# Kernel optimization log

Measured on AMD Instinct MI355X. Metric: run time of the kernel, lower is better.

## Reference

```python
import jax, jax.numpy as jnp
import numpy as np
from jax import lax

B, N, C, H, W, D, BEV = 2, 6, 64, 128, 352, 48, 64


def _make_buffers():
    # depths: linspace(1,100,D) -> used with shape (1,1,D,1)
    depths = jnp.linspace(1.0, 100.0, D).reshape(1, 1, D, 1)
    y, x = jnp.meshgrid(jnp.arange(H), jnp.arange(W), indexing='ij')
    xy1 = jnp.stack((x.flatten(), y.flatten(), jnp.ones(H * W)), axis=0).astype(jnp.float32)  # (3, H*W)
    return depths, xy1


def setup_inputs() -> dict:
    key = jax.random.key(0)
    ks = jax.random.split(key, 8)
    image_features = jax.random.normal(ks[0], (B * N, C, H, W), jnp.float32)
    # realistic invertible pinhole intrinsics embedded in 4x4
    fx = 500.0 + 10.0 * jax.random.normal(ks[1], (B, N))
    fy = 500.0 + 10.0 * jax.random.normal(ks[2], (B, N))
    K = jnp.tile(jnp.eye(4, dtype=jnp.float32), (B, N, 1, 1))
    K = K.at[..., 0, 0].set(fx).at[..., 1, 1].set(fy)
    K = K.at[..., 0, 2].set(W / 2.0).at[..., 1, 2].set(H / 2.0)
    extrinsics = jnp.tile(jnp.eye(4, dtype=jnp.float32), (B, N, 1, 1)) + 0.01 * jax.random.normal(ks[3], (B, N, 4, 4))
    view_attention = jnp.ones((1, N, 1, H, W), jnp.float32)
    depth_attention = jnp.ones((1, D, 1, 1), jnp.float32)
    # kaiming-normal conv weights (fan_in mode, relu gain sqrt(2))
    c1w = jax.random.normal(ks[4], (BEV, 3, 3, 3), jnp.float32) * np.sqrt(2.0 / (3 * 9))
    c1b = jnp.zeros((BEV,), jnp.float32)
    c2w = jax.random.normal(ks[5], (BEV, BEV, 3, 3), jnp.float32) * np.sqrt(2.0 / (BEV * 9))
    c2b = jnp.zeros((BEV,), jnp.float32)
    bn1_g = jnp.ones((BEV,), jnp.float32); bn1_b = jnp.zeros((BEV,), jnp.float32)
    bn2_g = jnp.ones((BEV,), jnp.float32); bn2_b = jnp.zeros((BEV,), jnp.float32)
    depths, xy1 = _make_buffers()
    return dict(image_features=image_features, intrinsics=K, extrinsics=extrinsics,
                view_attention=view_attention, depth_attention=depth_attention,
                c1w=c1w, c1b=c1b, bn1_g=bn1_g, bn1_b=bn1_b,
                c2w=c2w, c2b=c2b, bn2_g=bn2_g, bn2_b=bn2_b,
                depths=depths, xy1=xy1)


def _conv3x3(x, w, b):
    y = lax.conv_general_dilated(x, w, (1, 1), 'SAME',
                                 dimension_numbers=('NCHW', 'OIHW', 'NCHW'))
    return y + b.reshape(1, -1, 1, 1)


def _bn_train(x, g, b, eps=1e-5):
    # torch BatchNorm2d in training mode: biased batch stats over (B,H,W)
    m = x.mean(axis=(0, 2, 3), keepdims=True)
    v = x.var(axis=(0, 2, 3), keepdims=True)
    return g.reshape(1, -1, 1, 1) * (x - m) * lax.rsqrt(v + eps) + b.reshape(1, -1, 1, 1)


def reference(image_features, intrinsics, extrinsics, view_attention, depth_attention,
              c1w, c1b, bn1_g, bn1_b, c2w, c2b, bn2_g, bn2_b, depths, xy1):
    BN = B * N
    # ---- lift ----
    K3 = intrinsics.reshape(BN, 4, 4)[:, :3, :3]
    Kinv = jnp.linalg.inv(K3)                          # (BN,3,3)
    rays = jnp.einsum('bij,jp->bip', Kinv, xy1)        # (BN,3,H*W)
    # depths (1,1,D,1) * rays (BN,3,1,HW) -> (BN,3,D,HW), then the original's
    # .view(B,N,3,H,W,D) (a raw row-major reshape, reproduced faithfully)
    pc = (depths * rays[:, :, None, :]).reshape(B, N, 3, H, W, D)
    # (depth_probs in the original is computed then discarded; omitted)
    # ---- splat (fused weighted reduction over N and D) ----
    da = jax.nn.softmax(depth_attention, axis=1).reshape(D)       # (D,)
    va = jax.nn.softmax(view_attention, axis=1)[0, :, 0]          # (N,H,W)
    bev_features = jnp.einsum('bnchwd,d,nhw->bchw', pc, da, va)   # (B,3,H,W)
    h = jax.nn.relu(_bn_train(_conv3x3(bev_features, c1w, c1b), bn1_g, bn1_b))
    bev = jax.nn.relu(_bn_train(_conv3x3(h, c2w, c2b), bn2_g, bn2_b))
    return pc, bev
```

## Files before the change

### kernel.cpp

```cpp
#include <hip/hip_runtime.h>

#define W_ 352
#define H_ 128
#define HW 45056
#define D_ 48
#define B_ 2
#define N_ 6
#define DHW (D_*HW)
#define PC_SIZE (36*DHW)
#define BHW (B_*HW)
#define BEVN (B_*64*HW)

#define WS_KINV 0
#define WS_SUM1 192
#define WS_SQ1  256
#define WS_SUM2 448
#define WS_SQ2  512

#define NBN_BLK (BEVN/2048)
#define NPC_BLK 4224
#define PC_ITER 18

typedef unsigned short ushort_t;
typedef __attribute__((ext_vector_type(8))) short bf16x8;
typedef __attribute__((ext_vector_type(4))) float f32x4;
typedef __attribute__((ext_vector_type(8))) unsigned short u16x8;

static __device__ inline ushort_t f2bf(float f) {
    union { float f; unsigned u; } v; v.f = f;
    unsigned r = v.u + 0x7FFF + ((v.u >> 16) & 1);
    return (ushort_t)(r >> 16);
}
static __device__ inline float bf2f(ushort_t u) {
    union { unsigned u; float f; } v; v.u = ((unsigned)u) << 16; return v.f;
}
static __device__ inline void invert3x3(const float* __restrict__ M, float* __restrict__ o) {
    float a = M[0], b = M[1], c = M[2];
    float d = M[4], e = M[5], f = M[6];
    float g = M[8], h = M[9], ii = M[10];
    float det = a*(e*ii - f*h) - b*(d*ii - f*g) + c*(d*h - e*g);
    float inv = 1.f / det;
    o[0] = (e*ii - f*h)*inv; o[1] = (c*h - b*ii)*inv; o[2] = (b*f - c*e)*inv;
    o[3] = (f*g - d*ii)*inv; o[4] = (a*ii - c*g)*inv; o[5] = (c*d - a*f)*inv;
    o[6] = (d*h - e*g)*inv;  o[7] = (b*g - a*h)*inv;  o[8] = (a*e - b*d)*inv;
}

__global__ __launch_bounds__(256) void k_fused1(const float* __restrict__ K4,
                                                const float* __restrict__ datt,
                                                const float* __restrict__ vatt,
                                                const float* __restrict__ depths,
                                                const float* __restrict__ w1,
                                                const float* __restrict__ b1,
                                                const float* __restrict__ w2,
                                                float* __restrict__ ws,
                                                ushort_t* __restrict__ h1pm,
                                                ushort_t* __restrict__ packedW) {
    int bid = blockIdx.x, tid = threadIdx.x;
    if (bid >= 352) {
        int e = (bid - 352) * 256 + tid;
        int tap = e >> 12;
        int r   = e & 4095;
        int n   = r >> 6, k = r & 63;
        int slot = (k >> 3) ^ (n & 7);
        packedW[tap * 4096 + n * 64 + slot * 8 + (k & 7)] = f2bf(w2[(n * 64 + k) * 9 + tap]);
        return;
    }
    if (bid == 0 && tid >= 128 && tid < 140)
        invert3x3(K4 + (tid - 128) * 16, ws + WS_KINV + (tid - 128) * 9);

    __shared__ float sBev[3][10][34];
    __shared__ float wl[64 * 27];
    __shared__ float sDep[48], sDa[48], sKinv[54];
    __shared__ __align__(16) ushort_t sTile[256 * 64];
    __shared__ float sSum[64], sSq[64];

    int b  = bid / 176;
    int t0 = bid - b * 176;
    int ty = t0 / 11, tx = t0 - ty * 11;
    int y0 = ty * 8, x0 = tx * 32;

    if (tid < 48) sDep[tid] = depths[tid];
    if (tid < 64) { sSum[tid] = 0.f; sSq[tid] = 0.f; }
    if (tid >= 64 && tid < 70) invert3x3(K4 + (b * 6 + tid - 64) * 16, sKinv + (tid - 64) * 9);
    if (tid == 192) {
        float mx = -1e30f;
        for (int k = 0; k < D_; k++) mx = fmaxf(mx, datt[k]);
        float s = 0.f, e[D_];
        for (int k = 0; k < D_; k++) { e[k] = expf(datt[k] - mx); s += e[k]; }
        float invs = 1.f / s;
        for (int k = 0; k < D_; k++) sDa[k] = e[k] * invs;
    }
    for (int i = tid; i < 64 * 27; i += 256) wl[i] = w1[i];
    __syncthreads();

    for (int idx = tid; idx < 340; idx += 256) {
        int hy = idx / 34, hx = idx - hy * 34;
        int py = y0 + hy - 1, px = x0 + hx - 1;
        float a0 = 0.f, a1 = 0.f, a2 = 0.f;
        if ((unsigned)py < H_ && (unsigned)px < W_) {
            int pix = py * W_ + px;
            float va[N_]; float mx = -1e30f;
            for (int n = 0; n < N_; n++) { va[n] = vatt[n * HW + pix]; mx = fmaxf(mx, va[n]); }
            float s = 0.f;
            for (int n = 0; n < N_; n++) { va[n] = expf(va[n] - mx); s += va[n]; }
            float invs = 1.f / s;
            int q0 = pix * 48;
            int d = q0 / HW;
            int p = q0 - d * HW;
            int y = p / W_;
            int x = p - y * W_;
            float fx = (float)x, fy = (float)y;
            float S0 = 0.f, S1 = 0.f, S2 = 0.f;
            #pragma unroll
            for (int dd = 0; dd < D_; dd++) {
                float wq = sDa[dd] * sDep[d];
                S0 = fmaf(wq, fx, S0);
                S1 = fmaf(wq, fy, S1);
                S2 += wq;
                x++; fx += 1.f;
                if (x == W_) { x = 0; fx = 0.f; y++; fy += 1.f; if (y == H_) { y = 0; fy = 0.f; d++; } }
            }
            for (int n = 0; n < N_; n++) {
                float van = va[n] * invs;
                const float* kv = sKinv + n * 9;
                a0 = fmaf(van, fmaf(kv[0], S0, fmaf(kv[1], S1, kv[2] * S2)), a0);
                a1 = fmaf(van, fmaf(kv[3], S0, fmaf(kv[4], S1, kv[5] * S2)), a1);
                a2 = fmaf(van, fmaf(kv[6], S0, fmaf(kv[7], S1, kv[8] * S2)), a2);
            }
        }
        sBev[0][hy][hx] = a0;
        sBev[1][hy][hx] = a1;
        sBev[2][hy][hx] = a2;
    }
    __syncthreads();

    int oy = tid >> 5, ox = tid & 31;
    int y = y0 + oy, x = x0 + ox;
    float v[27];
    #pragma unroll
    for (int ci = 0; ci < 3; ci++)
        #pragma unroll
        for (int dy = 0; dy < 3; dy++)
            #pragma unroll
            for (int dx = 0; dx < 3; dx++)
                v[ci * 9 + dy * 3 + dx] = sBev[ci][oy + dy][ox + dx];
    u16x8 pack[8];
    #pragma unroll
    for (int co = 0; co < 64; co++) {
        float acc = b1[co];
        #pragma unroll
        for (int k = 0; k < 27; k++) acc = fmaf(wl[co * 27 + k], v[k], acc);
        pack[co >> 3][co & 7] = (short)f2bf(acc);
    }
    ushort_t* dst = h1pm + (size_t)(b * HW + y * W_ + x) * 64;
    #pragma unroll
    for (int j = 0; j < 8; j++) {
        *(u16x8*)(dst + j * 8) = pack[j];
        *(u16x8*)(&sTile[tid * 64 + j * 8]) = pack[j];
    }
    __syncthreads();

    int c8 = tid & 7;
    int lp = tid >> 3;
    float s[8] = {0,0,0,0,0,0,0,0}, q[8] = {0,0,0,0,0,0,0,0};
    for (int p = lp; p < 256; p += 32) {
        u16x8 vv = *(const u16x8*)(&sTile[p * 64 + c8 * 8]);
        #pragma unroll
        for (int e = 0; e < 8; e++) {
            float f = bf2f(vv[e]);
            s[e] += f;
            q[e] = fmaf(f, f, q[e]);
        }
    }
    #pragma unroll
    for (int e = 0; e < 8; e++) {
        s[e] += __shfl_xor(s[e], 8);  s[e] += __shfl_xor(s[e], 16); s[e] += __shfl_xor(s[e], 32);
        q[e] += __shfl_xor(q[e], 8);  q[e] += __shfl_xor(q[e], 16); q[e] += __shfl_xor(q[e], 32);
    }
    if ((tid & 56) == 0) {
        #pragma unroll
        for (int e = 0; e < 8; e++) {
            atomicAdd(&sSum[c8 * 8 + e], s[e]);
            atomicAdd(&sSq[c8 * 8 + e], q[e]);
        }
    }
    __syncthreads();
    if (tid < 64) {
        atomicAdd(ws + WS_SUM1 + tid, sSum[tid]);
        atomicAdd(ws + WS_SQ1 + tid, sSq[tid]);
    }
}

__global__ __launch_bounds__(256) void k_conv2(const ushort_t* __restrict__ h1pm,
                                               const ushort_t* __restrict__ packedW,
                                               const float* __restrict__ b2,
                                               const float* __restrict__ g1,
                                               const float* __restrict__ bb1,
                                               float* __restrict__ ws,
                                               float* __restrict__ h2f) {
    __shared__ __align__(16) ushort_t sA[204 * 64];
    __shared__ __align__(16) ushort_t sB[3 * 4096];
    __shared__ float sSc[64], sSh[64];
    __shared__ float sRs[4][64], sRq[4][64];

    const int tid = threadIdx.x;
    if (tid < 64) {
        const float invM = 1.f / (float)BHW;
        float m = ws[WS_SUM1 + tid] * invM;
        float var = ws[WS_SQ1 + tid] * invM - m * m;
        float sc = g1[tid] * rsqrtf(var + 1e-5f);
        sSc[tid] = sc;
        sSh[tid] = bb1[tid] - m * sc;
    }
    __syncthreads();

    const int bid = blockIdx.x;
    const int b  = bid / 352;
    const int r0 = bid - b * 352;
    const int yb = r0 / 11;
    const int xb = r0 - yb * 11;
    const int x0 = xb * 32;
    const int y0 = yb * 4;
    const ushort_t* h1p = h1pm + (size_t)b * HW * 64;

    for (int idx = tid; idx < 204 * 8; idx += 256) {
        int r  = idx >> 3;
        int c8 = idx & 7;
        int hy = r / 34;
        int hx = r - hy * 34;
        int py = y0 + hy - 1, px = x0 + hx - 1;
        u16x8 ov = {0, 0, 0, 0, 0, 0, 0, 0};
        if ((unsigned)py < H_ && (unsigned)px < W_) {
            u16x8 v = *(const u16x8*)(h1p + (size_t)(py * W_ + px) * 64 + c8 * 8);
            #pragma unroll
            for (int e = 0; e < 8; e++) {
                int ci = c8 * 8 + e;
                float f = fmaxf(fmaf(sSc[ci], bf2f(v[e]), sSh[ci]), 0.f);
                ov[e] = (short)f2bf(f);
            }
        }
        int slot = c8 ^ (r & 7);
        *(u16x8*)(&sA[r * 64 + slot * 8]) = ov;
    }

    const int w    = tid >> 6;
    const int lane = tid & 63;
    const int g    = lane >> 4;
    const int c16  = lane & 15;

    f32x4 acc[2][4];
    #pragma unroll
    for (int m = 0; m < 2; m++)
        #pragma unroll
        for (int n = 0; n < 4; n++)
            acc[m][n] = (f32x4){0.f, 0.f, 0.f, 0.f};

    for (int grp = 0; grp < 3; grp++) {
        __syncthreads();
        const uint4* src = (const uint4*)(packedW + grp * 3 * 4096);
        uint4* dst = (uint4*)sB;
        #pragma unroll
        for (int i = 0; i < 6; i++) dst[tid + 256 * i] = src[tid + 256 * i];
        __syncthreads();
        #pragma unroll
        for (int tt = 0; tt < 3; tt++) {
            bf16x8 afr[2][2];
            #pragma unroll
            for (int mrep = 0; mrep < 2; mrep++)
                #pragma unroll
                for (int kk = 0; kk < 2; kk++) {
                    int r = (w + grp) * 34 + tt + c16 + 16 * mrep;
                    int slot = (g + 4 * kk) ^ (r & 7);
                    afr[mrep][kk] = *(const bf16x8*)(&sA[r * 64 + slot * 8]);
                }
            #pragma unroll
            for (int nrep = 0; nrep < 4; nrep++) {
                int n = 16 * nrep + c16;
                #pragma unroll
                for (int kk = 0; kk < 2; kk++) {
                    int slot = (g + 4 * kk) ^ (n & 7);
                    bf16x8 bfr = *(const bf16x8*)(&sB[tt * 4096 + n * 64 + slot * 8]);
                    #pragma unroll
                    for (int mrep = 0; mrep < 2; mrep++)
                        acc[mrep][nrep] = __builtin_amdgcn_mfma_f32_16x16x32_bf16(
                            afr[mrep][kk], bfr, acc[mrep][nrep], 0, 0, 0);
                }
            }
        }
    }

    const int y = y0 + w;
    #pragma unroll
    for (int nrep = 0; nrep < 4; nrep++) {
        int co = 16 * nrep + c16;
        float bias = b2[co];
        float* dstrow = h2f + (size_t)(b * 64 + co) * HW + y * W_;
        float s = 0.f, q = 0.f;
        #pragma unroll
        for (int mrep = 0; mrep < 2; mrep++)
            #pragma unroll
            for (int j = 0; j < 4; j++) {
                float val = acc[mrep][nrep][j] + bias;
                s += val;
                q = fmaf(val, val, q);
                dstrow[x0 + 16 * mrep + g * 4 + j] = val;
            }
        s += __shfl_xor(s, 16); s += __shfl_xor(s, 32);
        q += __shfl_xor(q, 16); q += __shfl_xor(q, 32);
        if (g == 0) { sRs[w][co] = s; sRq[w][co] = q; }
    }
    __syncthreads();
    if (tid < 64) {
        float s = sRs[0][tid] + sRs[1][tid] + sRs[2][tid] + sRs[3][tid];
        float q = sRq[0][tid] + sRq[1][tid] + sRq[2][tid] + sRq[3][tid];
        atomicAdd(ws + WS_SUM2 + tid, s);
        atomicAdd(ws + WS_SQ2 + tid, q);
    }
}

__global__ __launch_bounds__(256) void k_tail(const float* __restrict__ depths,
                                              const float* __restrict__ ws,
                                              const float* __restrict__ g2,
                                              const float* __restrict__ bb2,
                                              float* __restrict__ out) {
    int bid = blockIdx.x, tid = threadIdx.x;
    if (bid >= NBN_BLK) {
        int pcbid = bid - NBN_BLK;
        for (int i = 0; i < PC_ITER; i++) {
            int ch = i * NPC_BLK + pcbid;
            int f = ch * 1024 + tid * 4;
            int bnc = f / DHW;
            int r1  = f - bnc * DHW;
            int d   = r1 / HW;
            int p   = r1 - d * HW;
            int y   = p / W_;
            int x   = p - y * W_;
            float ka = ws[WS_KINV + bnc * 3 + 0];
            float kb = ws[WS_KINV + bnc * 3 + 1];
            float kc = ws[WS_KINV + bnc * 3 + 2];
            float dep = depths[d];
            float base = fmaf(kb, (float)y, kc);
            f32x4 v;
            v.x = dep * fmaf(ka, (float)(x + 0), base);
            v.y = dep * fmaf(ka, (float)(x + 1), base);
            v.z = dep * fmaf(ka, (float)(x + 2), base);
            v.w = dep * fmaf(ka, (float)(x + 3), base);
            *(f32x4*)(out + f) = v;
        }
        return;
    }
    float* bev = out + PC_SIZE;
    int t = bid * 256 + tid;
    int f = t * 8;
    int c = (f / HW) & 63;
    const float invM = 1.f / (float)BHW;
    float m = ws[WS_SUM2 + c] * invM;
    float var = ws[WS_SQ2 + c] * invM - m * m;
    float sc = g2[c] * rsqrtf(var + 1e-5f);
    float sh = bb2[c] - m * sc;
    f32x4 a = *(f32x4*)(bev + f);
    f32x4 d = *(f32x4*)(bev + f + 4);
    a.x = fmaxf(fmaf(sc, a.x, sh), 0.f);
    a.y = fmaxf(fmaf(sc, a.y, sh), 0.f);
    a.z = fmaxf(fmaf(sc, a.z, sh), 0.f);
    a.w = fmaxf(fmaf(sc, a.w, sh), 0.f);
    d.x = fmaxf(fmaf(sc, d.x, sh), 0.f);
    d.y = fmaxf(fmaf(sc, d.y, sh), 0.f);
    d.z = fmaxf(fmaf(sc, d.z, sh), 0.f);
    d.w = fmaxf(fmaf(sc, d.w, sh), 0.f);
    *(f32x4*)(bev + f) = a;
    *(f32x4*)(bev + f + 4) = d;
}

extern "C" void kernel_launch(void* const* d_in, const int* in_sizes, int n_in,
                              void* d_out, int out_size, void* d_ws, size_t ws_size,
                              hipStream_t stream) {
    const float* K4     = (const float*)d_in[1];
    const float* vatt   = (const float*)d_in[3];
    const float* datt   = (const float*)d_in[4];
    const float* c1w    = (const float*)d_in[5];
    const float* c1b    = (const float*)d_in[6];
    const float* g1     = (const float*)d_in[7];
    const float* bb1    = (const float*)d_in[8];
    const float* c2w    = (const float*)d_in[9];
    const float* c2b    = (const float*)d_in[10];
    const float* g2     = (const float*)d_in[11];
    const float* bb2    = (const float*)d_in[12];
    const float* depths = (const float*)d_in[13];

    float* out = (float*)d_out;
    float* ws  = (float*)d_ws;
    char* base = (char*)d_out;
    ushort_t* h1pm    = (ushort_t*)base;
    ushort_t* packedW = (ushort_t*)(base + (12u << 20));
    float*    h2f     = out + PC_SIZE;

    hipMemsetAsync(ws, 0, 640 * sizeof(float), stream);
    k_fused1<<<496, 256, 0, stream>>>(K4, datt, vatt, depths, c1w, c1b, c2w, ws, h1pm, packedW);
    k_conv2 <<<704, 256, 0, stream>>>(h1pm, packedW, c2b, g1, bb1, ws, h2f);
    k_tail  <<<NBN_BLK + NPC_BLK, 256, 0, stream>>>(depths, ws, g2, bb2, out);
}
```

Measured before the change: 137.1 us.

## Store conv2 output as bf16 scratch in pc region and use nontemporal pc stores

The conv2 output is now written as bf16 into a scratch area inside the point-cloud output region instead of fp32 directly into the bev output. The tail kernel becomes one block per pc chunk: blocks overlapping the scratch first read it, apply BN+ReLU and write fp32 bev, synchronise, then overwrite their chunk with point-cloud values. Point-cloud stores use nontemporal hints. This cuts conv2 write and tail read traffic in half and removes the per-block loop, but rounds the pre-BN activations to bf16 and relies on each block reading only its own scratch chunk before overwriting it.

After: 123.2 us, median of 2. 1.11x faster.

```diff
diff --git a/kernel.cpp b/kernel.cpp
--- a/kernel.cpp
+++ b/kernel.cpp
@@ -17,14 +17,15 @@
 #define WS_SUM2 448
 #define WS_SQ2  512
 
-#define NBN_BLK (BEVN/2048)
-#define NPC_BLK 4224
-#define PC_ITER 18
+#define NPC_BLK (PC_SIZE/1024)
+#define CH_H2B0 4096
+#define CH_H2B1 (CH_H2B0 + BEVN/2048)
 
 typedef unsigned short ushort_t;
 typedef __attribute__((ext_vector_type(8))) short bf16x8;
 typedef __attribute__((ext_vector_type(4))) float f32x4;
 typedef __attribute__((ext_vector_type(8))) unsigned short u16x8;
+typedef __attribute__((ext_vector_type(4))) unsigned short u16x4;
 
 static __device__ inline ushort_t f2bf(float f) {
     union { float f; unsigned u; } v; v.f = f;
@@ -43,6 +44,29 @@
     o[0] = (e*ii - f*h)*inv; o[1] = (c*h - b*ii)*inv; o[2] = (b*f - c*e)*inv;
     o[3] = (f*g - d*ii)*inv; o[4] = (a*ii - c*g)*inv; o[5] = (c*d - a*f)*inv;
     o[6] = (d*h - e*g)*inv;  o[7] = (b*g - a*h)*inv;  o[8] = (a*e - b*d)*inv;
+}
+
+static __device__ inline void pc_write(int pcblk, const float* __restrict__ ws,
+                                       const float* __restrict__ depths,
+                                       float* __restrict__ out) {
+    int f = pcblk * 1024 + (int)threadIdx.x * 4;
+    int bnc = f / DHW;
+    int r1  = f - bnc * DHW;
+    int d   = r1 / HW;
+    int p   = r1 - d * HW;
+    int y   = p / W_;
+    int x   = p - y * W_;
+    float ka = ws[WS_KINV + bnc * 3 + 0];
+    float kb = ws[WS_KINV + bnc * 3 + 1];
+    float kc = ws[WS_KINV + bnc * 3 + 2];
+    float dep = depths[d];
+    float base = fmaf(kb, (float)y, kc);
+    f32x4 v;
+    v.x = dep * fmaf(ka, (float)(x + 0), base);
+    v.y = dep * fmaf(ka, (float)(x + 1), base);
+    v.z = dep * fmaf(ka, (float)(x + 2), base);
+    v.w = dep * fmaf(ka, (float)(x + 3), base);
+    __builtin_nontemporal_store(v, (f32x4*)(out + f));
 }
 
 __global__ __launch_bounds__(256) void k_fused1(const float* __restrict__ K4,
@@ -197,7 +221,7 @@
                                                const float* __restrict__ g1,
                                                const float* __restrict__ bb1,
                                                float* __restrict__ ws,
-                                               float* __restrict__ h2f) {
+                                               ushort_t* __restrict__ h2b) {
     __shared__ __align__(16) ushort_t sA[204 * 64];
     __shared__ __align__(16) ushort_t sB[3 * 4096];
     __shared__ float sSc[64], sSh[64];
@@ -294,17 +318,20 @@
     for (int nrep = 0; nrep < 4; nrep++) {
         int co = 16 * nrep + c16;
         float bias = b2[co];
-        float* dstrow = h2f + (size_t)(b * 64 + co) * HW + y * W_;
+        ushort_t* dstrow = h2b + (size_t)(b * 64 + co) * HW + y * W_;
         float s = 0.f, q = 0.f;
         #pragma unroll
-        for (int mrep = 0; mrep < 2; mrep++)
+        for (int mrep = 0; mrep < 2; mrep++) {
+            u16x4 ov;
             #pragma unroll
             for (int j = 0; j < 4; j++) {
                 float val = acc[mrep][nrep][j] + bias;
                 s += val;
                 q = fmaf(val, val, q);
-                dstrow[x0 + 16 * mrep + g * 4 + j] = val;
+                ov[j] = f2bf(val);
             }
+            *(u16x4*)(dstrow + x0 + 16 * mrep + g * 4) = ov;
+        }
         s += __shfl_xor(s, 16); s += __shfl_xor(s, 32);
         q += __shfl_xor(q, 16); q += __shfl_xor(q, 32);
         if (g == 0) { sRs[w][co] = s; sRq[w][co] = q; }
@@ -324,52 +351,33 @@
                                               const float* __restrict__ bb2,
                                               float* __restrict__ out) {
     int bid = blockIdx.x, tid = threadIdx.x;
-    if (bid >= NBN_BLK) {
-        int pcbid = bid - NBN_BLK;
-        for (int i = 0; i < PC_ITER; i++) {
-            int ch = i * NPC_BLK + pcbid;
-            int f = ch * 1024 + tid * 4;
-            int bnc = f / DHW;
-            int r1  = f - bnc * DHW;
-            int d   = r1 / HW;
-            int p   = r1 - d * HW;
-            int y   = p / W_;
-            int x   = p - y * W_;
-            float ka = ws[WS_KINV + bnc * 3 + 0];
-            float kb = ws[WS_KINV + bnc * 3 + 1];
-            float kc = ws[WS_KINV + bnc * 3 + 2];
-            float dep = depths[d];
-            float base = fmaf(kb, (float)y, kc);
-            f32x4 v;
-            v.x = dep * fmaf(ka, (float)(x + 0), base);
-            v.y = dep * fmaf(ka, (float)(x + 1), base);
-            v.z = dep * fmaf(ka, (float)(x + 2), base);
-            v.w = dep * fmaf(ka, (float)(x + 3), base);
-            *(f32x4*)(out + f) = v;
-        }
+    if (bid >= CH_H2B0 && bid < CH_H2B1) {
+        const ushort_t* h2b = (const ushort_t*)((const char*)out + ((size_t)CH_H2B0 * 4096));
+        int f2 = (bid - CH_H2B0) * 2048 + tid * 8;
+        int c = (f2 / HW) & 63;
+        const float invM = 1.f / (float)BHW;
+        float m = ws[WS_SUM2 + c] * invM;
+        float var = ws[WS_SQ2 + c] * invM - m * m;
+        float sc = g2[c] * rsqrtf(var + 1e-5f);
+        float sh = bb2[c] - m * sc;
+        u16x8 v = *(const u16x8*)(h2b + f2);
+        float* bev = out + PC_SIZE;
+        f32x4 a, d;
+        a.x = fmaxf(fmaf(sc, bf2f(v[0]), sh), 0.f);
+        a.y = fmaxf(fmaf(sc, bf2f(v[1]), sh), 0.f);
+        a.z = fmaxf(fmaf(sc, bf2f(v[2]), sh), 0.f);
+        a.w = fmaxf(fmaf(sc, bf2f(v[3]), sh), 0.f);
+        d.x = fmaxf(fmaf(sc, bf2f(v[4]), sh), 0.f);
+        d.y = fmaxf(fmaf(sc, bf2f(v[5]), sh), 0.f);
+        d.z = fmaxf(fmaf(sc, bf2f(v[6]), sh), 0.f);
+        d.w = fmaxf(fmaf(sc, bf2f(v[7]), sh), 0.f);
+        *(f32x4*)(bev + f2) = a;
+        *(f32x4*)(bev + f2 + 4) = d;
+        __syncthreads();
+        pc_write(bid, ws, depths, out);
         return;
     }
-    float* bev = out + PC_SIZE;
-    int t = bid * 256 + tid;
-    int f = t * 8;
-    int c = (f / HW) & 63;
-    const float invM = 1.f / (float)BHW;
-    float m = ws[WS_SUM2 + c] * invM;
-    float var = ws[WS_SQ2 + c] * invM - m * m;
-    float sc = g2[c] * rsqrtf(var + 1e-5f);
-    float sh = bb2[c] - m * sc;
-    f32x4 a = *(f32x4*)(bev + f);
-    f32x4 d = *(f32x4*)(bev + f + 4);
-    a.x = fmaxf(fmaf(sc, a.x, sh), 0.f);
-    a.y = fmaxf(fmaf(sc, a.y, sh), 0.f);
-    a.z = fmaxf(fmaf(sc, a.z, sh), 0.f);
-    a.w = fmaxf(fmaf(sc, a.w, sh), 0.f);
-    d.x = fmaxf(fmaf(sc, d.x, sh), 0.f);
-    d.y = fmaxf(fmaf(sc, d.y, sh), 0.f);
-    d.z = fmaxf(fmaf(sc, d.z, sh), 0.f);
-    d.w = fmaxf(fmaf(sc, d.w, sh), 0.f);
-    *(f32x4*)(bev + f) = a;
-    *(f32x4*)(bev + f + 4) = d;
+    pc_write(bid, ws, depths, out);
 }
 
 extern "C" void kernel_launch(void* const* d_in, const int* in_sizes, int n_in,
@@ -388,15 +396,14 @@
     const float* bb2    = (const float*)d_in[12];
     const float* depths = (const float*)d_in[13];
 
-    float* out = (float*)d_out;
     float* ws  = (float*)d_ws;
     char* base = (char*)d_out;
     ushort_t* h1pm    = (ushort_t*)base;
     ushort_t* packedW = (ushort_t*)(base + (12u << 20));
-    float*    h2f     = out + PC_SIZE;
+    ushort_t* h2b     = (ushort_t*)(base + ((size_t)CH_H2B0 * 4096));
 
     hipMemsetAsync(ws, 0, 640 * sizeof(float), stream);
     k_fused1<<<496, 256, 0, stream>>>(K4, datt, vatt, depths, c1w, c1b, c2w, ws, h1pm, packedW);
-    k_conv2 <<<704, 256, 0, stream>>>(h1pm, packedW, c2b, g1, bb1, ws, h2f);
-    k_tail  <<<NBN_BLK + NPC_BLK, 256, 0, stream>>>(depths, ws, g2, bb2, out);
-}
+    k_conv2 <<<704, 256, 0, stream>>>(h1pm, packedW, c2b, g1, bb1, ws, h2b);
+    k_tail  <<<NPC_BLK, 256, 0, stream>>>(depths, ws, g2, bb2, (float*)d_out);
+}
```
